# Kernel tuning notes

Hardware: AMD Instinct MI355X
Metric: run time of the kernel (lower is better)

The kernel has to match this reference:

```python
import jax, jax.numpy as jnp
import numpy as np

N_NODES = 50000
N_EDGES = 800000
IN_FEATS = 128
OUT_FEATS = 128
DROP_P = 0.5
BN_EPS = 1e-5


def setup_inputs() -> dict:
    key = jax.random.key(0)
    k_feat, k_src, k_dst, k_w, k_b, k_g, k_beta, k_mask = jax.random.split(key, 8)
    feat = jax.random.normal(k_feat, (N_NODES, IN_FEATS), dtype=jnp.float32)
    src = jax.random.randint(k_src, (N_EDGES,), 0, N_NODES, dtype=jnp.int32)
    dst = jax.random.randint(k_dst, (N_EDGES,), 0, N_NODES, dtype=jnp.int32)
    # GraphConv linear params (Glorot-ish scale)
    W = jax.random.normal(k_w, (IN_FEATS, OUT_FEATS), dtype=jnp.float32) / np.sqrt(IN_FEATS)
    b = jnp.zeros((OUT_FEATS,), dtype=jnp.float32)
    # BatchNorm1d affine params
    gamma = jnp.ones((OUT_FEATS,), dtype=jnp.float32)
    beta = jnp.zeros((OUT_FEATS,), dtype=jnp.float32)
    # Deterministic dropout keep-mask (Bernoulli(1-p)) as float 0/1
    drop_mask = (jax.random.uniform(k_mask, (N_NODES, OUT_FEATS)) >= DROP_P).astype(jnp.float32)
    return {"feat": feat, "src": src, "dst": dst, "W": W, "b": b,
            "gamma": gamma, "beta": beta, "drop_mask": drop_mask}


def _gcn_forward(feat, src, dst, W, b, gamma, beta, drop_mask):
    ones = jnp.ones((N_EDGES,), dtype=feat.dtype)
    deg_out = jax.ops.segment_sum(ones, src, num_segments=N_NODES)
    deg_in = jax.ops.segment_sum(ones, dst, num_segments=N_NODES)
    inv_sqrt_out = jnp.where(deg_out > 0, jax.lax.rsqrt(jnp.maximum(deg_out, 1.0)), 0.0)
    inv_sqrt_in = jnp.where(deg_in > 0, jax.lax.rsqrt(jnp.maximum(deg_in, 1.0)), 0.0)
    # norm='both': scale source features by out-degree^-1/2
    h = feat * inv_sqrt_out[:, None]                      # [N, F_in]
    # SpMM aggregation: sum messages from src into dst
    agg = jax.ops.segment_sum(h[src], dst, num_segments=N_NODES)  # [N, F_in]
    agg = agg * inv_sqrt_in[:, None]
    # Linear transform (W applied after aggregation; math-equivalent to DGL ordering)
    out = agg @ W + b                                      # [N, F_out]
    # Dropout (training mode, deterministic mask)
    out = out * drop_mask / (1.0 - DROP_P)
    # BatchNorm1d over the node dimension (training: batch stats, biased var)
    mean = jnp.mean(out, axis=0)
    var = jnp.var(out, axis=0)
    out = (out - mean) * jax.lax.rsqrt(var + BN_EPS) * gamma + beta
    return out


def reference(feat, src, dst, W, b, gamma, beta, drop_mask):
    return _gcn_forward(feat, src, dst, W, b, gamma, beta, drop_mask)
```

## Files before the change

kernel.cpp:

```cpp
#include <hip/hip_runtime.h>

#define NN 50000
#define NE 800000
#define F  128
#define BN_EPS 1e-5f
#define R    8
#define CAPR 16
#define CAP  (R * CAPR)

__global__ __launch_bounds__(256) void k_count_fill_rep(const int* __restrict__ src,
                                                        const int* __restrict__ dst,
                                                        int* __restrict__ degout_rep,
                                                        int* __restrict__ cursor,
                                                        int* __restrict__ bucket) {
    int i = blockIdx.x * 256 + threadIdx.x;
    int rep = blockIdx.x & (R - 1);
    if (i < NE) {
        int s = src[i];
        int d = dst[i];
        atomicAdd(&degout_rep[rep * NN + s], 1);
        int pos = atomicAdd(&cursor[rep * NN + d], 1);
        if (pos < CAPR) bucket[(size_t)d * CAP + rep * CAPR + pos] = s;
    }
}

__global__ __launch_bounds__(256) void k_invout(const int* __restrict__ degout_rep,
                                                float* __restrict__ inv_out) {
    int i = blockIdx.x * 256 + threadIdx.x;
    if (i < NN) {
        int t = 0;
        #pragma unroll
        for (int r = 0; r < R; ++r) t += degout_rep[r * NN + i];
        inv_out[i] = (t > 0) ? rsqrtf((float)t) : 0.0f;
    }
}

__global__ __launch_bounds__(256) void k_gather(const float4* __restrict__ feat4,
                                                const int* __restrict__ bucket,
                                                const int* __restrict__ cursor,
                                                const float* __restrict__ inv_out,
                                                float4* __restrict__ agg4) {
    int node = blockIdx.x * 8 + (threadIdx.x >> 5);
    int lane = threadIdx.x & 31;
    if (node >= NN) return;

    int cl = 0;
    if (lane < R) cl = min(cursor[lane * NN + node], CAPR);
    int c[R];
    int deg = 0;
    #pragma unroll
    for (int r = 0; r < R; ++r) { c[r] = __shfl(cl, r, 32); deg += c[r]; }

    const int* bkt = bucket + (size_t)node * CAP;
    float4 acc = make_float4(0.f, 0.f, 0.f, 0.f);

    for (int b = 0; b < deg; b += 32) {
        int n = min(32, deg - b);
        int sl = 0;
        float scl = 0.0f;
        if (lane < n) {
            int jj = b + lane;
            int rep = 0;
            #pragma unroll
            for (int r = 0; r < R - 1; ++r) {
                bool adv = (rep == r) && (jj >= c[r]);
                if (adv) { jj -= c[r]; rep = r + 1; }
            }
            sl  = bkt[rep * CAPR + jj];
            scl = inv_out[sl];
        }
        int j = 0;
        for (; j + 4 <= n; j += 4) {
            int s0 = __shfl(sl, j + 0, 32);
            int s1 = __shfl(sl, j + 1, 32);
            int s2 = __shfl(sl, j + 2, 32);
            int s3 = __shfl(sl, j + 3, 32);
            float c0 = __shfl(scl, j + 0, 32);
            float c1 = __shfl(scl, j + 1, 32);
            float c2 = __shfl(scl, j + 2, 32);
            float c3 = __shfl(scl, j + 3, 32);
            float4 v0 = feat4[(size_t)s0 * (F / 4) + lane];
            float4 v1 = feat4[(size_t)s1 * (F / 4) + lane];
            float4 v2 = feat4[(size_t)s2 * (F / 4) + lane];
            float4 v3 = feat4[(size_t)s3 * (F / 4) + lane];
            acc.x += v0.x * c0; acc.y += v0.y * c0; acc.z += v0.z * c0; acc.w += v0.w * c0;
            acc.x += v1.x * c1; acc.y += v1.y * c1; acc.z += v1.z * c1; acc.w += v1.w * c1;
            acc.x += v2.x * c2; acc.y += v2.y * c2; acc.z += v2.z * c2; acc.w += v2.w * c2;
            acc.x += v3.x * c3; acc.y += v3.y * c3; acc.z += v3.z * c3; acc.w += v3.w * c3;
        }
        for (; j < n; ++j) {
            int   s  = __shfl(sl, j, 32);
            float sc = __shfl(scl, j, 32);
            float4 v = feat4[(size_t)s * (F / 4) + lane];
            acc.x += v.x * sc; acc.y += v.y * sc;
            acc.z += v.z * sc; acc.w += v.w * sc;
        }
    }
    float si = (deg > 0) ? rsqrtf((float)deg) : 0.0f;
    acc.x *= si; acc.y *= si; acc.z *= si; acc.w *= si;
    agg4[(size_t)node * (F / 4) + lane] = acc;
}

__device__ __forceinline__ void fma4(float4& acc, float a, const float4& w) {
    acc.x += a * w.x; acc.y += a * w.y; acc.z += a * w.z; acc.w += a * w.w;
}

__global__ __launch_bounds__(128) void k_gemm(const float* __restrict__ agg,
                                              const float* __restrict__ W,
                                              const float* __restrict__ bias,
                                              const float* __restrict__ mask,
                                              float* __restrict__ out,
                                              float* __restrict__ colsum,
                                              float* __restrict__ colsumsq) {
    __shared__ float Wl[64 * F];
    __shared__ float s_sum[F];
    __shared__ float s_sq[F];

    int tid = threadIdx.x;
    const int cgrp = tid & 15;
    const int rgrp = tid >> 4;
    const int c0   = cgrp * 8;
    const int r0   = blockIdx.x * 64 + rgrp * 8;
    s_sum[tid] = 0.0f;
    s_sq[tid]  = 0.0f;

    const float4* agg4 = reinterpret_cast<const float4*>(agg);
    const float4* arow[8];
    #pragma unroll
    for (int i = 0; i < 8; ++i) {
        int r = r0 + i;
        arow[i] = agg4 + (size_t)((r < NN) ? r : 0) * (F / 4);
    }

    float4 acc[8][2];
    #pragma unroll
    for (int i = 0; i < 8; ++i) {
        acc[i][0] = make_float4(0.f, 0.f, 0.f, 0.f);
        acc[i][1] = make_float4(0.f, 0.f, 0.f, 0.f);
    }

    float4* Wl4w = reinterpret_cast<float4*>(Wl);
    const float4* Wl4 = reinterpret_cast<const float4*>(Wl);

    for (int half = 0; half < 2; ++half) {
        __syncthreads();
        const float4* Wg4 = reinterpret_cast<const float4*>(W + half * 64 * F);
        #pragma unroll
        for (int i = 0; i < 16; ++i)
            Wl4w[tid + i * 128] = Wg4[tid + i * 128];
        __syncthreads();

        #pragma unroll 2
        for (int k4 = 0; k4 < 16; ++k4) {
            float4 tv[8];
            #pragma unroll
            for (int i = 0; i < 8; ++i) tv[i] = arow[i][half * 16 + k4];
            #pragma unroll
            for (int kk = 0; kk < 4; ++kk) {
                const float4 w0 = Wl4[((k4 * 4 + kk) * F + c0) >> 2];
                const float4 w1 = Wl4[((k4 * 4 + kk) * F + c0 + 4) >> 2];
                #pragma unroll
                for (int i = 0; i < 8; ++i) {
                    float a = (&tv[i].x)[kk];
                    fma4(acc[i][0], a, w0);
                    fma4(acc[i][1], a, w1);
                }
            }
        }
    }

    float4 b0 = *reinterpret_cast<const float4*>(bias + c0);
    float4 b1 = *reinterpret_cast<const float4*>(bias + c0 + 4);
    float lsum[8] = {0, 0, 0, 0, 0, 0, 0, 0};
    float lsq[8]  = {0, 0, 0, 0, 0, 0, 0, 0};
    #pragma unroll
    for (int i = 0; i < 8; ++i) {
        int r = r0 + i;
        if (r < NN) {
            const float4* mrow = reinterpret_cast<const float4*>(mask + (size_t)r * F + c0);
            float4 m0 = mrow[0];
            float4 m1 = mrow[1];
            float4 o0, o1;
            o0.x = (acc[i][0].x + b0.x) * m0.x * 2.0f;
            o0.y = (acc[i][0].y + b0.y) * m0.y * 2.0f;
            o0.z = (acc[i][0].z + b0.z) * m0.z * 2.0f;
            o0.w = (acc[i][0].w + b0.w) * m0.w * 2.0f;
            o1.x = (acc[i][1].x + b1.x) * m1.x * 2.0f;
            o1.y = (acc[i][1].y + b1.y) * m1.y * 2.0f;
            o1.z = (acc[i][1].z + b1.z) * m1.z * 2.0f;
            o1.w = (acc[i][1].w + b1.w) * m1.w * 2.0f;
            float4* orow = reinterpret_cast<float4*>(out + (size_t)r * F + c0);
            orow[0] = o0;
            orow[1] = o1;
            lsum[0] += o0.x; lsq[0] += o0.x * o0.x;
            lsum[1] += o0.y; lsq[1] += o0.y * o0.y;
            lsum[2] += o0.z; lsq[2] += o0.z * o0.z;
            lsum[3] += o0.w; lsq[3] += o0.w * o0.w;
            lsum[4] += o1.x; lsq[4] += o1.x * o1.x;
            lsum[5] += o1.y; lsq[5] += o1.y * o1.y;
            lsum[6] += o1.z; lsq[6] += o1.z * o1.z;
            lsum[7] += o1.w; lsq[7] += o1.w * o1.w;
        }
    }
    #pragma unroll
    for (int j = 0; j < 8; ++j) {
        atomicAdd(&s_sum[c0 + j], lsum[j]);
        atomicAdd(&s_sq[c0 + j], lsq[j]);
    }
    __syncthreads();
    atomicAdd(&colsum[tid], s_sum[tid]);
    atomicAdd(&colsumsq[tid], s_sq[tid]);
}

__global__ __launch_bounds__(256) void k_bn(float4* __restrict__ out4,
                                            const float* __restrict__ colsum,
                                            const float* __restrict__ colsumsq,
                                            const float* __restrict__ gamma,
                                            const float* __restrict__ beta) {
    __shared__ float ssc[F];
    __shared__ float ssh[F];
    int tid = threadIdx.x;
    if (tid < F) {
        float mean = colsum[tid] * (1.0f / NN);
        float var  = colsumsq[tid] * (1.0f / NN) - mean * mean;
        float sc   = rsqrtf(var + BN_EPS) * gamma[tid];
        ssc[tid] = sc;
        ssh[tid] = beta[tid] - mean * sc;
    }
    __syncthreads();
    int gid = blockIdx.x * 256 + tid;
    if (gid < NN * F / 4) {
        const float4 sc4 = reinterpret_cast<const float4*>(ssc)[gid & 31];
        const float4 sh4 = reinterpret_cast<const float4*>(ssh)[gid & 31];
        float4 v = out4[gid];
        v.x = v.x * sc4.x + sh4.x;
        v.y = v.y * sc4.y + sh4.y;
        v.z = v.z * sc4.z + sh4.z;
        v.w = v.w * sc4.w + sh4.w;
        out4[gid] = v;
    }
}

extern "C" void kernel_launch(void* const* d_in, const int* in_sizes, int n_in,
                              void* d_out, int out_size, void* d_ws, size_t ws_size,
                              hipStream_t stream) {
    const float* feat  = (const float*)d_in[0];
    const int*   src   = (const int*)d_in[1];
    const int*   dst   = (const int*)d_in[2];
    const float* W     = (const float*)d_in[3];
    const float* bias  = (const float*)d_in[4];
    const float* gamma = (const float*)d_in[5];
    const float* beta  = (const float*)d_in[6];
    const float* mask  = (const float*)d_in[7];
    float* out = (float*)d_out;

    float* agg        = (float*)d_ws;
    int*   bucket     = (int*)(agg + (size_t)NN * F);
    int*   cursor     = bucket + (size_t)NN * CAP;
    int*   degout_rep = cursor + (size_t)R * NN;
    float* colsum     = (float*)(degout_rep + (size_t)R * NN);
    float* colsumsq   = colsum + F;
    float* inv_out    = colsumsq + F;

    hipMemsetAsync(cursor, 0, (2 * (size_t)R * NN + 2 * F) * sizeof(int), stream);

    k_count_fill_rep<<<(NE + 255) / 256, 256, 0, stream>>>(src, dst, degout_rep,
                                                           cursor, bucket);
    k_invout<<<(NN + 255) / 256, 256, 0, stream>>>(degout_rep, inv_out);
    k_gather<<<NN / 8, 256, 0, stream>>>((const float4*)feat, bucket, cursor,
                                         inv_out, (float4*)agg);
    k_gemm<<<(NN + 63) / 64, 128, 0, stream>>>(agg, W, bias, mask, out,
                                               colsum, colsumsq);
    k_bn<<<(NN * F / 4 + 255) / 256, 256, 0, stream>>>((float4*)out, colsum,
                                                       colsumsq, gamma, beta);
}
```

Before: 290.6 us.

## Build degree and bucket lists with LDS atomics per node range

Replaces the global-atomic edge binning kernel with a kernel where each block owns a 1024-node range and one of 8 edge chunks. It counts in-degree cursors and out-degree histograms with shared-memory atomics and writes the results straight to global memory, which drops most of the large memset. Each block now scans its whole edge chunk, so every edge is read once per node range (49 times), trading global atomic contention for repeated coalesced int4 reads.

```diff
diff --git a/kernel.cpp b/kernel.cpp
--- a/kernel.cpp
+++ b/kernel.cpp
@@ -7,20 +7,58 @@
 #define R    8
 #define CAPR 16
 #define CAP  (R * CAPR)
-
-__global__ __launch_bounds__(256) void k_count_fill_rep(const int* __restrict__ src,
-                                                        const int* __restrict__ dst,
-                                                        int* __restrict__ degout_rep,
-                                                        int* __restrict__ cursor,
-                                                        int* __restrict__ bucket) {
-    int i = blockIdx.x * 256 + threadIdx.x;
-    int rep = blockIdx.x & (R - 1);
-    if (i < NE) {
-        int s = src[i];
-        int d = dst[i];
-        atomicAdd(&degout_rep[rep * NN + s], 1);
-        int pos = atomicAdd(&cursor[rep * NN + d], 1);
-        if (pos < CAPR) bucket[(size_t)d * CAP + rep * CAPR + pos] = s;
+#define NPB  1024
+#define NRANGE 49
+#define CHUNK  (NE / R)
+#define CHUNK4 (CHUNK / 4)
+
+__global__ __launch_bounds__(1024) void k_build(const int4* __restrict__ src4,
+                                                const int4* __restrict__ dst4,
+                                                const int* __restrict__ src,
+                                                int* __restrict__ degout_rep,
+                                                int* __restrict__ cursor,
+                                                int* __restrict__ bucket) {
+    int c = blockIdx.x & (R - 1);
+    int r = blockIdx.x >> 3;
+    int base = r * NPB;
+    int tid = threadIdx.x;
+    __shared__ int lcur[NPB];
+    __shared__ int lhist[NPB];
+    lcur[tid] = 0;
+    lhist[tid] = 0;
+    __syncthreads();
+
+    const int q0 = c * CHUNK4;
+    for (int q = q0 + tid; q < q0 + CHUNK4; q += NPB) {
+        int4 dv = dst4[q];
+        int e = q * 4;
+        #pragma unroll
+        for (int k = 0; k < 4; ++k) {
+            int d = (&dv.x)[k];
+            unsigned rel = (unsigned)(d - base);
+            if (rel < NPB) {
+                int pos = atomicAdd(&lcur[rel], 1);
+                if (pos < CAPR) {
+                    int s = src[e + k];
+                    bucket[(size_t)d * CAP + c * CAPR + pos] = s;
+                }
+            }
+        }
+    }
+    for (int q = q0 + tid; q < q0 + CHUNK4; q += NPB) {
+        int4 sv = src4[q];
+        #pragma unroll
+        for (int k = 0; k < 4; ++k) {
+            int s = (&sv.x)[k];
+            unsigned rel = (unsigned)(s - base);
+            if (rel < NPB) atomicAdd(&lhist[rel], 1);
+        }
+    }
+    __syncthreads();
+    int node = base + tid;
+    if (node < NN) {
+        cursor[c * NN + node] = lcur[tid];
+        degout_rep[c * NN + node] = lhist[tid];
     }
 }
 
@@ -262,10 +300,10 @@
     float* colsumsq   = colsum + F;
     float* inv_out    = colsumsq + F;
 
-    hipMemsetAsync(cursor, 0, (2 * (size_t)R * NN + 2 * F) * sizeof(int), stream);
-
-    k_count_fill_rep<<<(NE + 255) / 256, 256, 0, stream>>>(src, dst, degout_rep,
-                                                           cursor, bucket);
+    hipMemsetAsync(colsum, 0, 2 * F * sizeof(float), stream);
+
+    k_build<<<NRANGE * R, NPB, 0, stream>>>((const int4*)src, (const int4*)dst,
+                                            src, degout_rep, cursor, bucket);
     k_invout<<<(NN + 255) / 256, 256, 0, stream>>>(degout_rep, inv_out);
     k_gather<<<NN / 8, 256, 0, stream>>>((const float4*)feat, bucket, cursor,
                                          inv_out, (float4*)agg);
```

After: 260.0 us. 1.12x faster.
